# Kernel optimization log

Hardware: AMD Instinct MI355X
Metric: run time of the kernel (lower is better)

Reference implementation:

```python
import jax, jax.numpy as jnp
import numpy as np

N_QUERY, N_BACKGND, DIM = 2048, 8192, 32


def setup_inputs() -> dict:
    key = jax.random.key(0)
    k0, k1, k2, k3 = jax.random.split(key, 4)
    x_backgnd = jax.random.normal(k0, (N_BACKGND, DIM), dtype=jnp.float32)
    y_backgnd = jax.random.normal(k1, (N_BACKGND,), dtype=jnp.float32)
    x_query = jax.random.normal(k2, (N_QUERY, DIM), dtype=jnp.float32)
    r = jax.random.uniform(k3, (N_QUERY, N_BACKGND), dtype=jnp.float32)
    sigma = jnp.array([0.1], dtype=jnp.float32)      # nn.Parameter init_sigma
    r_scale = jnp.array([3.0], dtype=jnp.float32)    # nn.Parameter init_r_scale
    w = jnp.ones((DIM,), dtype=jnp.float32)          # trainable weights matrix
    return {"x_backgnd": x_backgnd, "y_backgnd": y_backgnd, "x_query": x_query,
            "r": r, "sigma": sigma, "r_scale": r_scale, "w": w}


def reference(x_backgnd, y_backgnd, x_query, r, sigma, r_scale, w):
    # weighted Euclidean distance: ||(xq - xb) * w|| via the expansion trick,
    # avoiding the (n_query, n_backgnd, dim) difference tensor.
    xq = x_query * w           # (nq, d)
    xb = x_backgnd * w         # (nb, d)
    q2 = jnp.sum(xq * xq, axis=1, keepdims=True)        # (nq, 1)
    b2 = jnp.sum(xb * xb, axis=1)                        # (nb,)
    d2 = q2 + b2[None, :] - 2.0 * (xq @ xb.T)            # (nq, nb)
    dists = jnp.sqrt(jnp.maximum(d2, 0.0))
    # exp kernel with relationship bias, normalize, weighted sum
    k_vals = jnp.exp(-dists / sigma + r_scale * r)       # sigma, r_scale broadcast (1,)
    k_sum = jnp.sum(k_vals, axis=1, keepdims=True) + 1e-8
    weights = k_vals / k_sum
    y_pred = weights @ y_backgnd                          # (nq,)
    return y_pred
```

## Files before the change

### kernel.cpp

```cpp
#include <hip/hip_runtime.h>
#include <math.h>

#define NQ 2048
#define NB 8192
#define DIM 32

#define LOG2E 1.44269504088896340736f

typedef _Float16 half8 __attribute__((ext_vector_type(8)));
typedef float    f32x4 __attribute__((ext_vector_type(4)));

#define WS_ACC 0
#define WS_Q2  16448
#define WS_B2  24640
#define WS_XQH 57408
#define WS_XBH 188480

__global__ __launch_bounds__(256) void relnw_pre(
    const float* __restrict__ xq, const float* __restrict__ xb,
    const float* __restrict__ w,
    _Float16* __restrict__ XQh, _Float16* __restrict__ XBh,
    float* __restrict__ q2, float* __restrict__ b2,
    float* __restrict__ acc)
{
    const int tid = threadIdx.x;
    const int gi  = blockIdx.x * 256 + tid;
    if (gi < 2 * NQ) acc[gi] = 0.f;

    const int row = blockIdx.x * 64 + (tid >> 2);
    const int p   = tid & 3;
    if (row >= NQ + NB) return;

    const float* src; _Float16* dst; float* s2; float scale;
    if (row < NQ) { src = xq + (size_t)row * DIM;
                    dst = XQh + (size_t)row * DIM; s2 = q2 + row; scale = 1.f; }
    else          { int j = row - NQ;
                    src = xb + (size_t)j * DIM;
                    dst = XBh + (size_t)j * DIM;   s2 = b2 + j;   scale = -2.f; }

    const float4 xa  = ((const float4*)src)[p * 2];
    const float4 xbv = ((const float4*)src)[p * 2 + 1];
    const float4 wa  = ((const float4*)w)[p * 2];
    const float4 wb  = ((const float4*)w)[p * 2 + 1];
    const float xs[8]  = {xa.x, xa.y, xa.z, xa.w, xbv.x, xbv.y, xbv.z, xbv.w};
    const float ws_[8] = {wa.x, wa.y, wa.z, wa.w, wb.x, wb.y, wb.z, wb.w};

    half8 h;
    float s = 0.f;
#pragma unroll
    for (int c = 0; c < 8; ++c) {
        float t = xs[c] * ws_[c];
        _Float16 hh = (_Float16)t;
        float th = (float)hh;
        s = fmaf(th, th, s);
        h[c] = (_Float16)(th * scale);
    }
    *(half8*)(dst + p * 8) = h;

    s += __shfl_xor(s, 1, 64);
    s += __shfl_xor(s, 2, 64);
    if (p == 0) *s2 = s;
}

#define BT_PER_WAVE 16
#define BG_PER_WAVE (BT_PER_WAVE * 16)
#define RB 4

__global__ __launch_bounds__(256) void relnw_main(
    const _Float16* __restrict__ XQh,
    const _Float16* __restrict__ XBh,
    const float* __restrict__ q2,
    const float* __restrict__ b2,
    const float* __restrict__ yb,
    const float* __restrict__ r,
    const float* __restrict__ sigma,
    const float* __restrict__ rscale,
    float* __restrict__ acc)
{
    const int tid  = threadIdx.x;
    const int lane = tid & 63;
    const int wid  = tid >> 6;
    const int m    = lane & 15;
    const int quad = lane >> 4;

    const int q0     = blockIdx.y * 16;
    const int bstart = (blockIdx.x * 4 + wid) * BG_PER_WAVE;

    const float c1 = -LOG2E / sigma[0];
    const float c2 =  LOG2E * rscale[0];

    const half8 afrag = *(const half8*)(XQh + (size_t)(q0 + m) * DIM + quad * 8);

    float q2r[4];
#pragma unroll
    for (int g = 0; g < 4; ++g) q2r[g] = q2[q0 + quad * 4 + g];

    const _Float16* xbp = XBh + (size_t)(bstart + m) * DIM + quad * 8;

    const float* rbase[4];
#pragma unroll
    for (int g = 0; g < 4; ++g)
        rbase[g] = r + (size_t)(q0 + quad * 4 + g) * NB + bstart + m;

    float sk[4]  = {0.f, 0.f, 0.f, 0.f};
    float sky[4] = {0.f, 0.f, 0.f, 0.f};

    float rr[2][RB][4];
#pragma unroll
    for (int i = 0; i < RB; ++i)
#pragma unroll
        for (int g = 0; g < 4; ++g)
            rr[0][i][g] = rbase[g][i * 16];

#pragma unroll
    for (int bt = 0; bt < BT_PER_WAVE / RB; ++bt) {
        const int cur = bt & 1;
        if (bt + 1 < BT_PER_WAVE / RB) {
#pragma unroll
            for (int i = 0; i < RB; ++i)
#pragma unroll
                for (int g = 0; g < 4; ++g)
                    rr[cur ^ 1][i][g] = rbase[g][((bt + 1) * RB + i) * 16];
        }
#pragma unroll
        for (int i = 0; i < RB; ++i) {
            const int it = bt * RB + i;
            const int bc = bstart + it * 16 + m;
            const half8 bfrag = *(const half8*)(xbp + (size_t)it * 16 * DIM);
            const float yv  = yb[bc];
            const float b2v = b2[bc];

            f32x4 cin;
#pragma unroll
            for (int g = 0; g < 4; ++g) cin[g] = q2r[g] + b2v;

            f32x4 d2v = __builtin_amdgcn_mfma_f32_16x16x32_f16(
                afrag, bfrag, cin, 0, 0, 0);

#pragma unroll
            for (int g = 0; g < 4; ++g) {
                float d2 = fmaxf(d2v[g], 0.f);
                float dist = __builtin_amdgcn_sqrtf(d2);
                float e = fmaf(dist, c1, rr[cur][i][g] * c2);
                float k = __builtin_amdgcn_exp2f(e);
                sk[g] += k;
                sky[g] = fmaf(k, yv, sky[g]);
            }
        }
    }

#pragma unroll
    for (int off = 1; off <= 8; off <<= 1) {
#pragma unroll
        for (int g = 0; g < 4; ++g) {
            sk[g]  += __shfl_xor(sk[g],  off, 64);
            sky[g] += __shfl_xor(sky[g], off, 64);
        }
    }
    if (m == 0) {
#pragma unroll
        for (int g = 0; g < 4; ++g) {
            atomicAdd(acc + (q0 + quad * 4 + g),      sk[g]);
            atomicAdd(acc + NQ + (q0 + quad * 4 + g), sky[g]);
        }
    }
}

__global__ __launch_bounds__(256) void relnw_finalize(
    const float* __restrict__ acc, float* __restrict__ out)
{
    int q = blockIdx.x * 256 + threadIdx.x;
    if (q < NQ)
        out[q] = acc[NQ + q] / (acc[q] + 1e-8f);
}

extern "C" void kernel_launch(void* const* d_in, const int* in_sizes, int n_in,
                              void* d_out, int out_size, void* d_ws, size_t ws_size,
                              hipStream_t stream) {
    const float* xb     = (const float*)d_in[0];
    const float* yb     = (const float*)d_in[1];
    const float* xq     = (const float*)d_in[2];
    const float* r      = (const float*)d_in[3];
    const float* sigma  = (const float*)d_in[4];
    const float* rscale = (const float*)d_in[5];
    const float* w      = (const float*)d_in[6];
    float* out = (float*)d_out;

    char* ws = (char*)d_ws;
    float*    acc = (float*)(ws + WS_ACC);
    float*    q2  = (float*)(ws + WS_Q2);
    float*    b2  = (float*)(ws + WS_B2);
    _Float16* XQh = (_Float16*)(ws + WS_XQH);
    _Float16* XBh = (_Float16*)(ws + WS_XBH);

    relnw_pre<<<(NQ + NB) / 64, 256, 0, stream>>>(xq, xb, w, XQh, XBh, q2, b2, acc);

    dim3 grid(NB / (4 * BG_PER_WAVE), NQ / 16);
    relnw_main<<<grid, 256, 0, stream>>>(XQh, XBh, q2, b2, yb, r, sigma, rscale, acc);

    relnw_finalize<<<(NQ + 255) / 256, 256, 0, stream>>>(acc, out);
}
```

Baseline: 112.9 us.

## Swap MFMA operands so each lane loads contiguous r rows as float4

Transposes the MFMA output mapping by swapping the A and B operands, so each lane owns one query row and four consecutive background columns. Reads of r, y and b2 become contiguous float4 vector loads instead of scalar strided loads. A deeper prefetch ring (8 r tiles, 3 stages of fragments) is added, the cross-lane reduction shrinks to two shuffles per value, and occupancy is hinted to 2 blocks per CU. The larger register buffers may raise register pressure.

```diff
diff --git a/kernel.cpp b/kernel.cpp
--- a/kernel.cpp
+++ b/kernel.cpp
@@ -64,9 +64,8 @@
 
 #define BT_PER_WAVE 16
 #define BG_PER_WAVE (BT_PER_WAVE * 16)
-#define RB 4
 
-__global__ __launch_bounds__(256) void relnw_main(
+__global__ __launch_bounds__(256, 2) void relnw_main(
     const _Float16* __restrict__ XQh,
     const _Float16* __restrict__ XBh,
     const float* __restrict__ q2,
@@ -89,80 +88,69 @@
     const float c1 = -LOG2E / sigma[0];
     const float c2 =  LOG2E * rscale[0];
 
-    const half8 afrag = *(const half8*)(XQh + (size_t)(q0 + m) * DIM + quad * 8);
-
-    float q2r[4];
-#pragma unroll
-    for (int g = 0; g < 4; ++g) q2r[g] = q2[q0 + quad * 4 + g];
+    const half8 qfrag = *(const half8*)(XQh + (size_t)(q0 + m) * DIM + quad * 8);
+    const float q2s   = q2[q0 + m];
 
     const _Float16* xbp = XBh + (size_t)(bstart + m) * DIM + quad * 8;
+    const float*    rp  = r  + (size_t)(q0 + m) * NB + bstart + quad * 4;
+    const float*    ybp = yb + bstart + quad * 4;
+    const float*    b2p = b2 + bstart + quad * 4;
 
-    const float* rbase[4];
-#pragma unroll
-    for (int g = 0; g < 4; ++g)
-        rbase[g] = r + (size_t)(q0 + quad * 4 + g) * NB + bstart + m;
+    float sk = 0.f, sky = 0.f;
 
-    float sk[4]  = {0.f, 0.f, 0.f, 0.f};
-    float sky[4] = {0.f, 0.f, 0.f, 0.f};
-
-    float rr[2][RB][4];
-#pragma unroll
-    for (int i = 0; i < RB; ++i)
-#pragma unroll
-        for (int g = 0; g < 4; ++g)
-            rr[0][i][g] = rbase[g][i * 16];
+    f32x4 rrb[8];
+    half8 af[3];
+    f32x4 yv[3], bb[3];
 
 #pragma unroll
-    for (int bt = 0; bt < BT_PER_WAVE / RB; ++bt) {
-        const int cur = bt & 1;
-        if (bt + 1 < BT_PER_WAVE / RB) {
+    for (int i = 0; i < 2; ++i) {
+        af[i] = *(const half8*)(xbp + (size_t)i * 16 * DIM);
+        yv[i] = *(const f32x4*)(ybp + i * 16);
+        bb[i] = *(const f32x4*)(b2p + i * 16);
+    }
 #pragma unroll
-            for (int i = 0; i < RB; ++i)
-#pragma unroll
-                for (int g = 0; g < 4; ++g)
-                    rr[cur ^ 1][i][g] = rbase[g][((bt + 1) * RB + i) * 16];
-        }
-#pragma unroll
-        for (int i = 0; i < RB; ++i) {
-            const int it = bt * RB + i;
-            const int bc = bstart + it * 16 + m;
-            const half8 bfrag = *(const half8*)(xbp + (size_t)it * 16 * DIM);
-            const float yv  = yb[bc];
-            const float b2v = b2[bc];
-
-            f32x4 cin;
-#pragma unroll
-            for (int g = 0; g < 4; ++g) cin[g] = q2r[g] + b2v;
-
-            f32x4 d2v = __builtin_amdgcn_mfma_f32_16x16x32_f16(
-                afrag, bfrag, cin, 0, 0, 0);
+    for (int i = 0; i < 8; ++i)
+        rrb[i] = *(const f32x4*)(rp + i * 16);
 
 #pragma unroll
-            for (int g = 0; g < 4; ++g) {
-                float d2 = fmaxf(d2v[g], 0.f);
-                float dist = __builtin_amdgcn_sqrtf(d2);
-                float e = fmaf(dist, c1, rr[cur][i][g] * c2);
-                float k = __builtin_amdgcn_exp2f(e);
-                sk[g] += k;
-                sky[g] = fmaf(k, yv, sky[g]);
-            }
+    for (int it = 0; it < 16; ++it) {
+        const int cs = it % 3;
+        const int ns = (it + 2) % 3;
+        if (it + 2 < 16) {
+            af[ns] = *(const half8*)(xbp + (size_t)(it + 2) * 16 * DIM);
+            yv[ns] = *(const f32x4*)(ybp + (it + 2) * 16);
+            bb[ns] = *(const f32x4*)(b2p + (it + 2) * 16);
         }
+
+        f32x4 cin;
+#pragma unroll
+        for (int g = 0; g < 4; ++g) cin[g] = q2s + bb[cs][g];
+
+        f32x4 d2v = __builtin_amdgcn_mfma_f32_16x16x32_f16(
+            af[cs], qfrag, cin, 0, 0, 0);
+
+        const int rs = it & 7;
+#pragma unroll
+        for (int g = 0; g < 4; ++g) {
+            float d2   = fmaxf(d2v[g], 0.f);
+            float dist = __builtin_amdgcn_sqrtf(d2);
+            float e    = fmaf(dist, c1, rrb[rs][g] * c2);
+            float k    = __builtin_amdgcn_exp2f(e);
+            sk += k;
+            sky = fmaf(k, yv[cs][g], sky);
+        }
+
+        if (it + 8 < 16)
+            rrb[rs] = *(const f32x4*)(rp + (it + 8) * 16);
     }
 
-#pragma unroll
-    for (int off = 1; off <= 8; off <<= 1) {
-#pragma unroll
-        for (int g = 0; g < 4; ++g) {
-            sk[g]  += __shfl_xor(sk[g],  off, 64);
-            sky[g] += __shfl_xor(sky[g], off, 64);
-        }
-    }
-    if (m == 0) {
-#pragma unroll
-        for (int g = 0; g < 4; ++g) {
-            atomicAdd(acc + (q0 + quad * 4 + g),      sk[g]);
-            atomicAdd(acc + NQ + (q0 + quad * 4 + g), sky[g]);
-        }
+    sk  += __shfl_xor(sk, 16, 64);
+    sk  += __shfl_xor(sk, 32, 64);
+    sky += __shfl_xor(sky, 16, 64);
+    sky += __shfl_xor(sky, 32, 64);
+    if (lane < 16) {
+        atomicAdd(acc + (q0 + m),      sk);
+        atomicAdd(acc + NQ + (q0 + m), sky);
     }
 }
 
```

After: 117.9 us. +4.5%, slower.
